# Optimization experiments

Measured on AMD Instinct MI355X. Metric: run time of the kernel, lower is better.

## Reference

```python
import jax, jax.numpy as jnp
import numpy as np

B, L, D = 2, 2048, 768
HEADS, KEY, HEAD = 12, 64, 64


def _glorot(key, shape):
    fan_in, fan_out = shape[0], shape[1]
    lim = jnp.sqrt(6.0 / (fan_in + fan_out))
    return jax.random.uniform(key, shape, jnp.float32, -lim, lim)


def setup_inputs() -> dict:
    key = jax.random.key(0)
    ks = jax.random.split(key, 8)
    return {
        "q": jax.random.normal(ks[0], (B, L, D), jnp.float32),
        "k": jax.random.normal(ks[1], (B, L, D), jnp.float32),
        "v": jax.random.normal(ks[2], (B, L, D), jnp.float32),
        "att_mask": jnp.ones((B, L), jnp.float32),
        "Wq": _glorot(ks[3], (D, HEADS * KEY)),
        "bq": jnp.zeros((HEADS * KEY,), jnp.float32),
        "Wk": _glorot(ks[4], (D, HEADS * KEY)),
        "bk": jnp.zeros((HEADS * KEY,), jnp.float32),
        "Wv": _glorot(ks[5], (D, HEADS * HEAD)),
        "bv": jnp.zeros((HEADS * HEAD,), jnp.float32),
        "Wo": _glorot(ks[6], (HEADS * HEAD, HEADS * HEAD)),
        "bo": jnp.zeros((HEADS * HEAD,), jnp.float32),
    }


def reference(q, k, v, att_mask, Wq, bq, Wk, bk, Wv, bv, Wo, bo):
    b, lq, _ = q.shape
    lk = k.shape[1]
    # att_mask [B,Lk] -> [B,Lq,Lk] via ones outer product (as in the TF code)
    mask2d = jnp.ones((b, lq, 1), jnp.float32) * att_mask[:, None, :]
    qh = (q @ Wq + bq).reshape(b, lq, HEADS, KEY)
    kh = (k @ Wk + bk).reshape(b, lk, HEADS, KEY)
    vh = (v @ Wv + bv).reshape(b, lk, HEADS, HEAD)
    # scores [B,H,Lq,Lk]
    a = jnp.einsum('binh,bjnh->bnij', qh, kh) / (KEY ** 0.5)
    a = a + (1.0 - mask2d[:, None, :, :]) * -99999.0
    a = jax.nn.softmax(a, axis=-1)
    o = jnp.einsum('bnij,bjnh->binh', a, vh).reshape(b, lq, HEADS * HEAD)
    return o @ Wo + bo
```

## Files before the change

### kernel.cpp

```cpp
#include <hip/hip_runtime.h>
#include <math.h>

#define BB 2
#define LL 2048
#define DD 768
#define NH 12
#define HD 64
#define QT 64
#define KT 32
#define NTILES (LL/KT)
#define EL (4096*768)
#define WEL (768*768)

typedef __attribute__((ext_vector_type(8))) short short8;
typedef __attribute__((ext_vector_type(4))) float f32x4;
typedef unsigned short ushortT;

union U8 { unsigned short u[8]; short8 v; };

#define MFMA(a,b,c) __builtin_amdgcn_mfma_f32_16x16x32_bf16((a),(b),(c),0,0,0)

__device__ inline unsigned short f2bf(float x) {
    unsigned int u = __float_as_uint(x);
    unsigned int r = (u + 0x7fffu + ((u >> 16) & 1u)) >> 16;
    return (unsigned short)r;
}
__device__ inline float bf2f(unsigned short s) {
    return __uint_as_float(((unsigned int)s) << 16);
}
__device__ inline void split2(float x, unsigned short& h, unsigned short& l) {
    h = f2bf(x);
    l = f2bf(x - bf2f(h));
}
__device__ inline int swz(int row) { return (((row & 7) ^ ((row >> 3) & 7)) << 4); }

__device__ inline void gl2lds16(const void* g, void* l) {
    __builtin_amdgcn_global_load_lds((__attribute__((address_space(1))) const void*)g,
                                     (__attribute__((address_space(3))) void*)l, 16, 0, 0);
}

struct SplitArgs { const float* src[3]; ushortT* dh[3]; ushortT* dl[3]; };
__global__ __launch_bounds__(256) void split_plain(SplitArgs a)
{
    const int z = blockIdx.y;
    const size_t i = ((size_t)blockIdx.x * 256 + threadIdx.x) * 8;
    const float* s = a.src[z];
    float4 v0 = *reinterpret_cast<const float4*>(s + i);
    float4 v1 = *reinterpret_cast<const float4*>(s + i + 4);
    float f[8] = {v0.x, v0.y, v0.z, v0.w, v1.x, v1.y, v1.z, v1.w};
    U8 h, l;
    #pragma unroll
    for (int j = 0; j < 8; ++j) split2(f[j], h.u[j], l.u[j]);
    *reinterpret_cast<short8*>(a.dh[z] + i) = h.v;
    *reinterpret_cast<short8*>(a.dl[z] + i) = l.v;
}

struct WArgs { const float* src[4]; ushortT* dh[4]; ushortT* dl[4]; };
__global__ __launch_bounds__(256) void split_wt(WArgs a)
{
    const int n  = blockIdx.x * 256 + threadIdx.x;
    const int k0 = blockIdx.y * 8;
    const int z  = blockIdx.z;
    const float* W = a.src[z];
    U8 h, l;
    #pragma unroll
    for (int j = 0; j < 8; ++j) {
        float x = W[(size_t)(k0 + j) * DD + n];
        split2(x, h.u[j], l.u[j]);
    }
    *reinterpret_cast<short8*>(a.dh[z] + (size_t)n * DD + k0) = h.v;
    *reinterpret_cast<short8*>(a.dl[z] + (size_t)n * DD + k0) = l.v;
}

template<int MODE>
__global__ __launch_bounds__(256) void gemm_mfma(const ushortT* __restrict__ Ah, size_t apb,
                                                 const ushortT* __restrict__ Bth, size_t bpb,
                                                 const float* __restrict__ bias,
                                                 float* __restrict__ outF,
                                                 ushortT* __restrict__ outH,
                                                 ushortT* __restrict__ outL)
{
    __shared__ ushortT As[64 * 64];
    __shared__ ushortT Bs[64 * 64];

    const int tid  = threadIdx.x;
    const int lane = tid & 63;
    const int w    = tid >> 6;
    const int g    = lane >> 4, c = lane & 15;
    const int n0   = blockIdx.x * 64;
    const int m0   = blockIdx.y * 64;

    const int srow0 = w * 16 + (lane >> 3);
    const int csrc  = (lane & 7) ^ (lane >> 3);
    const size_t plA = (csrc >= 4) ? apb : 0;
    const size_t plB = (csrc >= 4) ? bpb : 0;
    const size_t abase = (size_t)(m0 + srow0) * (DD * 2) + plA + (size_t)(csrc & 3) * 16;
    const size_t bbase = (size_t)(n0 + srow0) * (DD * 2) + plB + (size_t)(csrc & 3) * 16;

    f32x4 acc[4] = {{0,0,0,0},{0,0,0,0},{0,0,0,0},{0,0,0,0}};

    const int arow = w * 16 + c;
    const int ar7  = arow & 7;
    const int ahc  = g ^ ar7;
    const int aoff_h = arow * 64 + ahc * 8;
    const int aoff_l = arow * 64 + (ahc ^ 4) * 8;

    for (int kt = 0; kt < DD / 32; ++kt) {
        const size_t ko = (size_t)kt * 64;
        const char* asrc = (const char*)Ah  + abase + ko;
        const char* bsrc = (const char*)Bth + bbase + ko;
        gl2lds16(asrc,            &As[w * 1024]);
        gl2lds16(asrc + 8 * (DD * 2), &As[w * 1024 + 512]);
        gl2lds16(bsrc,            &Bs[w * 1024]);
        gl2lds16(bsrc + 8 * (DD * 2), &Bs[w * 1024 + 512]);
        __syncthreads();

        const short8 a_h = *reinterpret_cast<const short8*>(&As[aoff_h]);
        const short8 a_l = *reinterpret_cast<const short8*>(&As[aoff_l]);
        #pragma unroll
        for (int nf = 0; nf < 4; ++nf) {
            const int brow = nf * 16 + c;
            const int bhc  = g ^ (brow & 7);
            const short8 b_h = *reinterpret_cast<const short8*>(&Bs[brow * 64 + bhc * 8]);
            const short8 b_l = *reinterpret_cast<const short8*>(&Bs[brow * 64 + (bhc ^ 4) * 8]);
            acc[nf] = MFMA(a_h, b_h, acc[nf]);
            acc[nf] = MFMA(a_l, b_h, acc[nf]);
            acc[nf] = MFMA(a_h, b_l, acc[nf]);
        }
        __syncthreads();
    }

    #pragma unroll
    for (int nf = 0; nf < 4; ++nf) {
        const int n = n0 + nf * 16 + c;
        const float bz = bias[n];
        #pragma unroll
        for (int r = 0; r < 4; ++r) {
            const int m = m0 + w * 16 + 4 * g + r;
            const float vv = acc[nf][r] + bz;
            if (MODE == 0) {
                outF[(size_t)m * DD + n] = vv;
            } else {
                unsigned short hh, ll;
                split2(vv, hh, ll);
                outH[(size_t)m * DD + n] = hh;
                outL[(size_t)m * DD + n] = ll;
            }
        }
    }
}

__global__ __launch_bounds__(256) void attn_mfma(const ushortT* __restrict__ Qh_g,
                                                 const ushortT* __restrict__ Ql_g,
                                                 const ushortT* __restrict__ Kh_g,
                                                 const ushortT* __restrict__ Kl_g,
                                                 const ushortT* __restrict__ Vh_g,
                                                 const ushortT* __restrict__ Vl_g,
                                                 const float* __restrict__ mask,
                                                 ushortT* __restrict__ Oh_g,
                                                 ushortT* __restrict__ Ol_g)
{
    __shared__ unsigned short Kh[32 * 64];
    __shared__ unsigned short Kl[32 * 64];
    __shared__ unsigned short Vt[64 * 64];
    __shared__ unsigned short Pb[4 * 16 * 64];
    __shared__ float mterm[KT];

    const int tid = threadIdx.x;
    const int l   = tid & 63;
    const int w   = tid >> 6;
    const int g   = l >> 4;
    const int c   = l & 15;
    const int bh  = blockIdx.y;
    const int b   = bh / NH;
    const int h   = bh % NH;
    const int r0  = blockIdx.x * QT;

    short8 qh[2], ql[2];
    {
        const size_t qoff = (size_t)(b * LL + r0 + w * 16 + c) * DD + h * 64 + 8 * g;
        qh[0] = *reinterpret_cast<const short8*>(Qh_g + qoff);
        qh[1] = *reinterpret_cast<const short8*>(Qh_g + qoff + 32);
        ql[0] = *reinterpret_cast<const short8*>(Ql_g + qoff);
        ql[1] = *reinterpret_cast<const short8*>(Ql_g + qoff + 32);
    }

    f32x4 Oa[4] = {{0,0,0,0},{0,0,0,0},{0,0,0,0},{0,0,0,0}};
    float mrun[4] = {-1e30f,-1e30f,-1e30f,-1e30f};
    float lrun[4] = {0.f,0.f,0.f,0.f};

    const int skey = tid >> 3;
    const int sd0  = (tid & 7) * 8;

    for (int kt = 0; kt < NTILES; ++kt) {
        __syncthreads();
        {
            const size_t ko = (size_t)(b * LL + kt * KT + skey) * DD + h * 64 + sd0;
            const short8 hh = *reinterpret_cast<const short8*>(Kh_g + ko);
            const short8 lo = *reinterpret_cast<const short8*>(Kl_g + ko);
            const int idx = skey * 64 + (((sd0 * 2) ^ swz(skey)) >> 1);
            *reinterpret_cast<short8*>(&Kh[idx]) = hh;
            *reinterpret_cast<short8*>(&Kl[idx]) = lo;
        }
        {
            const size_t vo = (size_t)(b * LL + kt * KT + skey) * DD + h * 64 + sd0;
            U8 vh8, vl8;
            vh8.v = *reinterpret_cast<const short8*>(Vh_g + vo);
            vl8.v = *reinterpret_cast<const short8*>(Vl_g + vo);
            #pragma unroll
            for (int j = 0; j < 8; ++j) {
                const int d = sd0 + j;
                const int s = swz(d);
                Vt[d * 64 + (((2 * skey) ^ s) >> 1)]      = vh8.u[j];
                Vt[d * 64 + (((64 + 2 * skey) ^ s) >> 1)] = vl8.u[j];
            }
        }
        if (tid < KT)
            mterm[tid] = (1.0f - mask[(size_t)b * LL + kt * KT + tid]) * -99999.0f;
        __syncthreads();

        f32x4 s[2];
        #pragma unroll
        for (int th = 0; th < 2; ++th) {
            const int row = th * 16 + c;
            const int sw = swz(row);
            const short8 kh0 = *reinterpret_cast<const short8*>(&Kh[row * 64 + (((16 * g     ) ^ sw) >> 1)]);
            const short8 kh1 = *reinterpret_cast<const short8*>(&Kh[row * 64 + (((16 * g + 64) ^ sw) >> 1)]);
            const short8 kl0 = *reinterpret_cast<const short8*>(&Kl[row * 64 + (((16 * g     ) ^ sw) >> 1)]);
            const short8 kl1 = *reinterpret_cast<const short8*>(&Kl[row * 64 + (((16 * g + 64) ^ sw) >> 1)]);
            f32x4 a = {0,0,0,0};
            a = MFMA(qh[0], kh0, a); a = MFMA(qh[1], kh1, a);
            a = MFMA(ql[0], kh0, a); a = MFMA(ql[1], kh1, a);
            a = MFMA(qh[0], kl0, a); a = MFMA(qh[1], kl1, a);
            const float mt = mterm[th * 16 + c];
            #pragma unroll
            for (int r = 0; r < 4; ++r) a[r] = fmaf(a[r], 0.125f, mt);
            s[th] = a;
        }

        float pexp[2][4];
        #pragma unroll
        for (int r = 0; r < 4; ++r) {
            float tm = fmaxf(s[0][r], s[1][r]);
            #pragma unroll
            for (int o = 1; o < 16; o <<= 1) tm = fmaxf(tm, __shfl_xor(tm, o));
            const float mn = fmaxf(mrun[r], tm);
            const float scale = __expf(mrun[r] - mn);
            const float p0 = __expf(s[0][r] - mn);
            const float p1 = __expf(s[1][r] - mn);
            float rs = p0 + p1;
            #pragma unroll
            for (int o = 1; o < 16; o <<= 1) rs += __shfl_xor(rs, o);
            lrun[r] = lrun[r] * scale + rs;
            mrun[r] = mn;
            pexp[0][r] = p0; pexp[1][r] = p1;
            #pragma unroll
            for (int n = 0; n < 4; ++n) Oa[n][r] *= scale;
        }

        unsigned short* Pw = &Pb[w * 16 * 64];
        #pragma unroll
        for (int th = 0; th < 2; ++th)
            #pragma unroll
            for (int r = 0; r < 4; ++r) {
                const int row = 4 * g + r;
                const int sw2 = swz(row);
                unsigned short h_, l_;
                split2(pexp[th][r], h_, l_);
                const int keyb = 2 * (th * 16 + c);
                Pw[row * 64 + ((keyb ^ sw2) >> 1)]        = h_;
                Pw[row * 64 + (((64 + keyb) ^ sw2) >> 1)] = l_;
            }
        asm volatile("s_waitcnt lgkmcnt(0)" ::: "memory");

        {
            const int sw2 = swz(c);
            const short8 pa_h = *reinterpret_cast<const short8*>(&Pw[c * 64 + (((16 * g     ) ^ sw2) >> 1)]);
            const short8 pa_l = *reinterpret_cast<const short8*>(&Pw[c * 64 + (((64 + 16 * g) ^ sw2) >> 1)]);
            #pragma unroll
            for (int n = 0; n < 4; ++n) {
                const int vrow = 16 * n + c;
                const int sv = swz(vrow);
                const short8 vh = *reinterpret_cast<const short8*>(&Vt[vrow * 64 + (((16 * g     ) ^ sv) >> 1)]);
                const short8 vl = *reinterpret_cast<const short8*>(&Vt[vrow * 64 + (((64 + 16 * g) ^ sv) >> 1)]);
                Oa[n] = MFMA(pa_h, vh, Oa[n]);
                Oa[n] = MFMA(pa_h, vl, Oa[n]);
                Oa[n] = MFMA(pa_l, vh, Oa[n]);
            }
        }
    }

    #pragma unroll
    for (int r = 0; r < 4; ++r) {
        const float inv = 1.0f / lrun[r];
        const int row = b * LL + r0 + w * 16 + 4 * g + r;
        ushortT* oh = Oh_g + (size_t)row * DD + h * 64;
        ushortT* ol = Ol_g + (size_t)row * DD + h * 64;
        #pragma unroll
        for (int n = 0; n < 4; ++n) {
            unsigned short hh, ll;
            split2(Oa[n][r] * inv, hh, ll);
            oh[16 * n + c] = hh;
            ol[16 * n + c] = ll;
        }
    }
}

extern "C" void kernel_launch(void* const* d_in, const int* in_sizes, int n_in,
                              void* d_out, int out_size, void* d_ws, size_t ws_size,
                              hipStream_t stream)
{
    const float* q    = (const float*)d_in[0];
    const float* k    = (const float*)d_in[1];
    const float* v    = (const float*)d_in[2];
    const float* amask= (const float*)d_in[3];
    const float* Wq   = (const float*)d_in[4];
    const float* bq   = (const float*)d_in[5];
    const float* Wk   = (const float*)d_in[6];
    const float* bk   = (const float*)d_in[7];
    const float* Wv   = (const float*)d_in[8];
    const float* bv   = (const float*)d_in[9];
    const float* Wo   = (const float*)d_in[10];
    const float* bo   = (const float*)d_in[11];
    float* out = (float*)d_out;

    ushortT* W0 = (ushortT*)d_ws;
    ushortT* qh = W0;            ushortT* ql = W0 + (size_t)EL;
    ushortT* kh = W0 + 2*(size_t)EL;  ushortT* kl = W0 + 3*(size_t)EL;
    ushortT* vh = W0 + 4*(size_t)EL;  ushortT* vl = W0 + 5*(size_t)EL;
    ushortT* wb = W0 + 6*(size_t)EL;
    ushortT* wqh = wb;            ushortT* wql = wb + (size_t)WEL;
    ushortT* wkh = wb + 2*(size_t)WEL; ushortT* wkl = wb + 3*(size_t)WEL;
    ushortT* wvh = wb + 4*(size_t)WEL; ushortT* wvl = wb + 5*(size_t)WEL;
    ushortT* woh = wb + 6*(size_t)WEL; ushortT* wol = wb + 7*(size_t)WEL;
    ushortT* pb = wb + 8*(size_t)WEL;
    ushortT* Qph = pb;            ushortT* Qpl = pb + (size_t)EL;
    ushortT* Kph = pb + 2*(size_t)EL;  ushortT* Kpl = pb + 3*(size_t)EL;
    ushortT* Vph = pb + 4*(size_t)EL;  ushortT* Vpl = pb + 5*(size_t)EL;
    ushortT* Oh = W0;             ushortT* Ol = W0 + (size_t)EL;

    const size_t APB = (size_t)EL * 2;
    const size_t WPB = (size_t)WEL * 2;

    SplitArgs sa;
    sa.src[0] = q; sa.src[1] = k; sa.src[2] = v;
    sa.dh[0] = qh; sa.dh[1] = kh; sa.dh[2] = vh;
    sa.dl[0] = ql; sa.dl[1] = kl; sa.dl[2] = vl;
    split_plain<<<dim3(EL / 2048, 3), 256, 0, stream>>>(sa);

    WArgs wa;
    wa.src[0] = Wq; wa.src[1] = Wk; wa.src[2] = Wv; wa.src[3] = Wo;
    wa.dh[0] = wqh; wa.dh[1] = wkh; wa.dh[2] = wvh; wa.dh[3] = woh;
    wa.dl[0] = wql; wa.dl[1] = wkl; wa.dl[2] = wvl; wa.dl[3] = wol;
    split_wt<<<dim3(3, 96, 4), 256, 0, stream>>>(wa);

    dim3 ggrid(DD / 64, 4096 / 64);
    gemm_mfma<1><<<ggrid, 256, 0, stream>>>(qh, APB, wqh, WPB, bq, nullptr, Qph, Qpl);
    gemm_mfma<1><<<ggrid, 256, 0, stream>>>(kh, APB, wkh, WPB, bk, nullptr, Kph, Kpl);
    gemm_mfma<1><<<ggrid, 256, 0, stream>>>(vh, APB, wvh, WPB, bv, nullptr, Vph, Vpl);

    dim3 agrid(LL / QT, BB * NH);
    attn_mfma<<<agrid, 256, 0, stream>>>(Qph, Qpl, Kph, Kpl, Vph, Vpl, amask, Oh, Ol);

    gemm_mfma<0><<<ggrid, 256, 0, stream>>>(Oh, APB, woh, WPB, bo, out, nullptr, nullptr);
}
```

Before: 410.7 us.

## Rewrite attention with 32x32 MFMA, register-resident P, and fold softmax scale into Wq

The attention kernel now uses 32x32x16 bf16 MFMA with two waves of 32 query rows each. The probability matrix stays in registers and is redistributed with lane shuffles instead of being staged through LDS. K tiles are loaded directly into LDS with global_load_lds, and the 1/sqrt(d) factor is folded into the Wq split and the bq bias, which removes the per-score scale. Each block now has fewer threads (128), which can lower occupancy and latency hiding, and per-lane register use for the accumulators grows.

```diff
diff --git a/kernel.cpp b/kernel.cpp
--- a/kernel.cpp
+++ b/kernel.cpp
@@ -6,19 +6,20 @@
 #define DD 768
 #define NH 12
 #define HD 64
-#define QT 64
-#define KT 32
-#define NTILES (LL/KT)
 #define EL (4096*768)
 #define WEL (768*768)
 
 typedef __attribute__((ext_vector_type(8))) short short8;
 typedef __attribute__((ext_vector_type(4))) float f32x4;
+typedef __attribute__((ext_vector_type(16))) float f32x16;
+typedef __attribute__((ext_vector_type(4))) unsigned int u32x4;
 typedef unsigned short ushortT;
 
 union U8 { unsigned short u[8]; short8 v; };
-
-#define MFMA(a,b,c) __builtin_amdgcn_mfma_f32_16x16x32_bf16((a),(b),(c),0,0,0)
+union UB { u32x4 u; short8 v; };
+
+#define MFMA(a,b,c)   __builtin_amdgcn_mfma_f32_16x16x32_bf16((a),(b),(c),0,0,0)
+#define MFMA32(a,b,c) __builtin_amdgcn_mfma_f32_32x32x16_bf16((a),(b),(c),0,0,0)
 
 __device__ inline unsigned short f2bf(float x) {
     unsigned int u = __float_as_uint(x);
@@ -55,17 +56,18 @@
     *reinterpret_cast<short8*>(a.dl[z] + i) = l.v;
 }
 
-struct WArgs { const float* src[4]; ushortT* dh[4]; ushortT* dl[4]; };
+struct WArgs { const float* src[4]; ushortT* dh[4]; ushortT* dl[4]; float scale[4]; };
 __global__ __launch_bounds__(256) void split_wt(WArgs a)
 {
     const int n  = blockIdx.x * 256 + threadIdx.x;
     const int k0 = blockIdx.y * 8;
     const int z  = blockIdx.z;
     const float* W = a.src[z];
+    const float sc = a.scale[z];
     U8 h, l;
     #pragma unroll
     for (int j = 0; j < 8; ++j) {
-        float x = W[(size_t)(k0 + j) * DD + n];
+        float x = W[(size_t)(k0 + j) * DD + n] * sc;
         split2(x, h.u[j], l.u[j]);
     }
     *reinterpret_cast<short8*>(a.dh[z] + (size_t)n * DD + k0) = h.v;
@@ -75,7 +77,7 @@
 template<int MODE>
 __global__ __launch_bounds__(256) void gemm_mfma(const ushortT* __restrict__ Ah, size_t apb,
                                                  const ushortT* __restrict__ Bth, size_t bpb,
-                                                 const float* __restrict__ bias,
+                                                 const float* __restrict__ bias, float bscale,
                                                  float* __restrict__ outF,
                                                  ushortT* __restrict__ outH,
                                                  ushortT* __restrict__ outL)
@@ -100,8 +102,7 @@
     f32x4 acc[4] = {{0,0,0,0},{0,0,0,0},{0,0,0,0},{0,0,0,0}};
 
     const int arow = w * 16 + c;
-    const int ar7  = arow & 7;
-    const int ahc  = g ^ ar7;
+    const int ahc  = g ^ (arow & 7);
     const int aoff_h = arow * 64 + ahc * 8;
     const int aoff_l = arow * 64 + (ahc ^ 4) * 8;
 
@@ -109,9 +110,9 @@
         const size_t ko = (size_t)kt * 64;
         const char* asrc = (const char*)Ah  + abase + ko;
         const char* bsrc = (const char*)Bth + bbase + ko;
-        gl2lds16(asrc,            &As[w * 1024]);
+        gl2lds16(asrc,                &As[w * 1024]);
         gl2lds16(asrc + 8 * (DD * 2), &As[w * 1024 + 512]);
-        gl2lds16(bsrc,            &Bs[w * 1024]);
+        gl2lds16(bsrc,                &Bs[w * 1024]);
         gl2lds16(bsrc + 8 * (DD * 2), &Bs[w * 1024 + 512]);
         __syncthreads();
 
@@ -133,7 +134,7 @@
     #pragma unroll
     for (int nf = 0; nf < 4; ++nf) {
         const int n = n0 + nf * 16 + c;
-        const float bz = bias[n];
+        const float bz = bias[n] * bscale;
         #pragma unroll
         for (int r = 0; r < 4; ++r) {
             const int m = m0 + w * 16 + 4 * g + r;
@@ -150,7 +151,7 @@
     }
 }
 
-__global__ __launch_bounds__(256) void attn_mfma(const ushortT* __restrict__ Qh_g,
+__global__ __launch_bounds__(128) void attn_mfma(const ushortT* __restrict__ Qh_g,
                                                  const ushortT* __restrict__ Ql_g,
                                                  const ushortT* __restrict__ Kh_g,
                                                  const ushortT* __restrict__ Kl_g,
@@ -160,150 +161,163 @@
                                                  ushortT* __restrict__ Oh_g,
                                                  ushortT* __restrict__ Ol_g)
 {
-    __shared__ unsigned short Kh[32 * 64];
-    __shared__ unsigned short Kl[32 * 64];
-    __shared__ unsigned short Vt[64 * 64];
-    __shared__ unsigned short Pb[4 * 16 * 64];
-    __shared__ float mterm[KT];
-
-    const int tid = threadIdx.x;
-    const int l   = tid & 63;
-    const int w   = tid >> 6;
-    const int g   = l >> 4;
-    const int c   = l & 15;
-    const int bh  = blockIdx.y;
-    const int b   = bh / NH;
-    const int h   = bh % NH;
-    const int r0  = blockIdx.x * QT;
-
-    short8 qh[2], ql[2];
+    __shared__ ushortT Kh[32 * 64];
+    __shared__ ushortT Kl[32 * 64];
+    __shared__ ushortT Vt[64 * 64];
+    __shared__ float mterm[32];
+
+    const int tid  = threadIdx.x;
+    const int lane = tid & 63;
+    const int w    = tid >> 6;
+    const int qc   = lane & 31;
+    const int h5   = lane >> 5;
+    const int bh   = blockIdx.y;
+    const int b    = bh / NH;
+    const int h    = bh % NH;
+    const int r0   = blockIdx.x * 64;
+    const int qrow = r0 + w * 32 + qc;
+
+    short8 qbh[4], qbl[4];
     {
-        const size_t qoff = (size_t)(b * LL + r0 + w * 16 + c) * DD + h * 64 + 8 * g;
-        qh[0] = *reinterpret_cast<const short8*>(Qh_g + qoff);
-        qh[1] = *reinterpret_cast<const short8*>(Qh_g + qoff + 32);
-        ql[0] = *reinterpret_cast<const short8*>(Ql_g + qoff);
-        ql[1] = *reinterpret_cast<const short8*>(Ql_g + qoff + 32);
-    }
-
-    f32x4 Oa[4] = {{0,0,0,0},{0,0,0,0},{0,0,0,0},{0,0,0,0}};
-    float mrun[4] = {-1e30f,-1e30f,-1e30f,-1e30f};
-    float lrun[4] = {0.f,0.f,0.f,0.f};
-
-    const int skey = tid >> 3;
-    const int sd0  = (tid & 7) * 8;
-
-    for (int kt = 0; kt < NTILES; ++kt) {
+        const size_t qoff = (size_t)(b * LL + qrow) * DD + h * 64;
+        #pragma unroll
+        for (int ks = 0; ks < 4; ++ks) {
+            const int d0 = 8 * h5 + 16 * ks;
+            qbh[ks] = *reinterpret_cast<const short8*>(Qh_g + qoff + d0);
+            qbl[ks] = *reinterpret_cast<const short8*>(Ql_g + qoff + d0);
+        }
+    }
+
+    f32x16 Oa[2];
+    #pragma unroll
+    for (int m = 0; m < 2; ++m)
+        #pragma unroll
+        for (int r = 0; r < 16; ++r) Oa[m][r] = 0.f;
+    float mrun = -1e30f, lrun = 0.f;
+
+    const int skey = tid >> 2;
+    const int sd0v = (tid & 3) * 16;
+    ushortT* kdst = w ? Kl : Kh;
+    const ushortT* ksrcp = w ? Kl_g : Kh_g;
+    const int krow_l = lane >> 3;
+    const int kcsrc  = (lane & 7) ^ krow_l;
+
+    for (int kt = 0; kt < LL / 32; ++kt) {
         __syncthreads();
         {
-            const size_t ko = (size_t)(b * LL + kt * KT + skey) * DD + h * 64 + sd0;
-            const short8 hh = *reinterpret_cast<const short8*>(Kh_g + ko);
-            const short8 lo = *reinterpret_cast<const short8*>(Kl_g + ko);
-            const int idx = skey * 64 + (((sd0 * 2) ^ swz(skey)) >> 1);
-            *reinterpret_cast<short8*>(&Kh[idx]) = hh;
-            *reinterpret_cast<short8*>(&Kl[idx]) = lo;
+            const size_t kbase = (size_t)(b * LL + kt * 32 + krow_l) * DD + h * 64 + kcsrc * 8;
+            #pragma unroll
+            for (int t = 0; t < 4; ++t)
+                gl2lds16(ksrcp + kbase + (size_t)(8 * t) * DD, kdst + t * 512);
         }
         {
-            const size_t vo = (size_t)(b * LL + kt * KT + skey) * DD + h * 64 + sd0;
-            U8 vh8, vl8;
-            vh8.v = *reinterpret_cast<const short8*>(Vh_g + vo);
-            vl8.v = *reinterpret_cast<const short8*>(Vl_g + vo);
+            const size_t vo = (size_t)(b * LL + kt * 32 + skey) * DD + h * 64 + sd0v;
+            U8 a0, a1, b0, b1;
+            a0.v = *reinterpret_cast<const short8*>(Vh_g + vo);
+            a1.v = *reinterpret_cast<const short8*>(Vh_g + vo + 8);
+            b0.v = *reinterpret_cast<const short8*>(Vl_g + vo);
+            b1.v = *reinterpret_cast<const short8*>(Vl_g + vo + 8);
             #pragma unroll
             for (int j = 0; j < 8; ++j) {
-                const int d = sd0 + j;
-                const int s = swz(d);
-                Vt[d * 64 + (((2 * skey) ^ s) >> 1)]      = vh8.u[j];
-                Vt[d * 64 + (((64 + 2 * skey) ^ s) >> 1)] = vl8.u[j];
+                int d = sd0v + j; int s = swz(d);
+                Vt[d * 64 + (((2 * skey) ^ s) >> 1)]      = a0.u[j];
+                Vt[d * 64 + (((64 + 2 * skey) ^ s) >> 1)] = b0.u[j];
+                d = sd0v + 8 + j; s = swz(d);
+                Vt[d * 64 + (((2 * skey) ^ s) >> 1)]      = a1.u[j];
+                Vt[d * 64 + (((64 + 2 * skey) ^ s) >> 1)] = b1.u[j];
             }
         }
-        if (tid < KT)
-            mterm[tid] = (1.0f - mask[(size_t)b * LL + kt * KT + tid]) * -99999.0f;
+        if (tid < 32)
+            mterm[tid] = (1.0f - mask[(size_t)b * LL + kt * 32 + tid]) * -99999.0f;
         __syncthreads();
 
-        f32x4 s[2];
-        #pragma unroll
-        for (int th = 0; th < 2; ++th) {
-            const int row = th * 16 + c;
-            const int sw = swz(row);
-            const short8 kh0 = *reinterpret_cast<const short8*>(&Kh[row * 64 + (((16 * g     ) ^ sw) >> 1)]);
-            const short8 kh1 = *reinterpret_cast<const short8*>(&Kh[row * 64 + (((16 * g + 64) ^ sw) >> 1)]);
-            const short8 kl0 = *reinterpret_cast<const short8*>(&Kl[row * 64 + (((16 * g     ) ^ sw) >> 1)]);
-            const short8 kl1 = *reinterpret_cast<const short8*>(&Kl[row * 64 + (((16 * g + 64) ^ sw) >> 1)]);
-            f32x4 a = {0,0,0,0};
-            a = MFMA(qh[0], kh0, a); a = MFMA(qh[1], kh1, a);
-            a = MFMA(ql[0], kh0, a); a = MFMA(ql[1], kh1, a);
-            a = MFMA(qh[0], kl0, a); a = MFMA(qh[1], kl1, a);
-            const float mt = mterm[th * 16 + c];
+        f32x16 sa;
+        #pragma unroll
+        for (int r = 0; r < 16; ++r) sa[r] = 0.f;
+        #pragma unroll
+        for (int ks = 0; ks < 4; ++ks) {
+            const int ch = (h5 + 2 * ks) ^ (qc & 7);
+            const short8 kfh = *reinterpret_cast<const short8*>(&Kh[qc * 64 + ch * 8]);
+            const short8 kfl = *reinterpret_cast<const short8*>(&Kl[qc * 64 + ch * 8]);
+            sa = MFMA32(kfh, qbh[ks], sa);
+            sa = MFMA32(kfl, qbh[ks], sa);
+            sa = MFMA32(kfh, qbl[ks], sa);
+        }
+
+        float sm[16];
+        #pragma unroll
+        for (int r = 0; r < 16; ++r)
+            sm[r] = sa[r] + mterm[(r & 3) + 8 * (r >> 2) + 4 * h5];
+        float tm = sm[0];
+        #pragma unroll
+        for (int r = 1; r < 16; ++r) tm = fmaxf(tm, sm[r]);
+        tm = fmaxf(tm, __shfl_xor(tm, 32));
+        const float mn = fmaxf(mrun, tm);
+        const float scale = __expf(mrun - mn);
+        float p[16];
+        float rs = 0.f;
+        #pragma unroll
+        for (int r = 0; r < 16; ++r) { p[r] = __expf(sm[r] - mn); rs += p[r]; }
+        rs += __shfl_xor(rs, 32);
+        lrun = lrun * scale + rs;
+        mrun = mn;
+        #pragma unroll
+        for (int m = 0; m < 2; ++m)
             #pragma unroll
-            for (int r = 0; r < 4; ++r) a[r] = fmaf(a[r], 0.125f, mt);
-            s[th] = a;
-        }
-
-        float pexp[2][4];
-        #pragma unroll
-        for (int r = 0; r < 4; ++r) {
-            float tm = fmaxf(s[0][r], s[1][r]);
+            for (int r = 0; r < 16; ++r) Oa[m][r] *= scale;
+
+        unsigned int pkh[8], pkl[8], xph[8], xpl[8];
+        #pragma unroll
+        for (int s2 = 0; s2 < 8; ++s2) {
+            unsigned short h0, l0, h1, l1;
+            split2(p[2 * s2],     h0, l0);
+            split2(p[2 * s2 + 1], h1, l1);
+            pkh[s2] = (unsigned int)h0 | ((unsigned int)h1 << 16);
+            pkl[s2] = (unsigned int)l0 | ((unsigned int)l1 << 16);
+            xph[s2] = __shfl_xor(pkh[s2], 32);
+            xpl[s2] = __shfl_xor(pkl[s2], 32);
+        }
+        UB pbh[2], pbl[2];
+        if (h5 == 0) {
+            pbh[0].u = (u32x4){pkh[0], pkh[1], xph[0], xph[1]};
+            pbl[0].u = (u32x4){pkl[0], pkl[1], xpl[0], xpl[1]};
+            pbh[1].u = (u32x4){pkh[4], pkh[5], xph[4], xph[5]};
+            pbl[1].u = (u32x4){pkl[4], pkl[5], xpl[4], xpl[5]};
+        } else {
+            pbh[0].u = (u32x4){xph[2], xph[3], pkh[2], pkh[3]};
+            pbl[0].u = (u32x4){xpl[2], xpl[3], pkl[2], pkl[3]};
+            pbh[1].u = (u32x4){xph[6], xph[7], pkh[6], pkh[7]};
+            pbl[1].u = (u32x4){xpl[6], xpl[7], pkl[6], pkl[7]};
+        }
+
+        #pragma unroll
+        for (int m = 0; m < 2; ++m) {
+            const int d  = qc + 32 * m;
+            const int sv = swz(d);
             #pragma unroll
-            for (int o = 1; o < 16; o <<= 1) tm = fmaxf(tm, __shfl_xor(tm, o));
-            const float mn = fmaxf(mrun[r], tm);
-            const float scale = __expf(mrun[r] - mn);
-            const float p0 = __expf(s[0][r] - mn);
-            const float p1 = __expf(s[1][r] - mn);
-            float rs = p0 + p1;
-            #pragma unroll
-            for (int o = 1; o < 16; o <<= 1) rs += __shfl_xor(rs, o);
-            lrun[r] = lrun[r] * scale + rs;
-            mrun[r] = mn;
-            pexp[0][r] = p0; pexp[1][r] = p1;
-            #pragma unroll
-            for (int n = 0; n < 4; ++n) Oa[n][r] *= scale;
-        }
-
-        unsigned short* Pw = &Pb[w * 16 * 64];
-        #pragma unroll
-        for (int th = 0; th < 2; ++th)
-            #pragma unroll
-            for (int r = 0; r < 4; ++r) {
-                const int row = 4 * g + r;
-                const int sw2 = swz(row);
-                unsigned short h_, l_;
-                split2(pexp[th][r], h_, l_);
-                const int keyb = 2 * (th * 16 + c);
-                Pw[row * 64 + ((keyb ^ sw2) >> 1)]        = h_;
-                Pw[row * 64 + (((64 + keyb) ^ sw2) >> 1)] = l_;
+            for (int ks2 = 0; ks2 < 2; ++ks2) {
+                const int bc = 16 * h5 + 32 * ks2;
+                const short8 vfh = *reinterpret_cast<const short8*>(&Vt[d * 64 + ((bc ^ sv) >> 1)]);
+                const short8 vfl = *reinterpret_cast<const short8*>(&Vt[d * 64 + (((64 + bc) ^ sv) >> 1)]);
+                Oa[m] = MFMA32(vfh, pbh[ks2].v, Oa[m]);
+                Oa[m] = MFMA32(vfl, pbh[ks2].v, Oa[m]);
+                Oa[m] = MFMA32(vfh, pbl[ks2].v, Oa[m]);
             }
-        asm volatile("s_waitcnt lgkmcnt(0)" ::: "memory");
-
-        {
-            const int sw2 = swz(c);
-            const short8 pa_h = *reinterpret_cast<const short8*>(&Pw[c * 64 + (((16 * g     ) ^ sw2) >> 1)]);
-            const short8 pa_l = *reinterpret_cast<const short8*>(&Pw[c * 64 + (((64 + 16 * g) ^ sw2) >> 1)]);
-            #pragma unroll
-            for (int n = 0; n < 4; ++n) {
-                const int vrow = 16 * n + c;
-                const int sv = swz(vrow);
-                const short8 vh = *reinterpret_cast<const short8*>(&Vt[vrow * 64 + (((16 * g     ) ^ sv) >> 1)]);
-                const short8 vl = *reinterpret_cast<const short8*>(&Vt[vrow * 64 + (((64 + 16 * g) ^ sv) >> 1)]);
-                Oa[n] = MFMA(pa_h, vh, Oa[n]);
-                Oa[n] = MFMA(pa_h, vl, Oa[n]);
-                Oa[n] = MFMA(pa_l, vh, Oa[n]);
-            }
-        }
-    }
-
-    #pragma unroll
-    for (int r = 0; r < 4; ++r) {
-        const float inv = 1.0f / lrun[r];
-        const int row = b * LL + r0 + w * 16 + 4 * g + r;
-        ushortT* oh = Oh_g + (size_t)row * DD + h * 64;
-        ushortT* ol = Ol_g + (size_t)row * DD + h * 64;
-        #pragma unroll
-        for (int n = 0; n < 4; ++n) {
+        }
+    }
+
+    const float inv = 1.0f / lrun;
+    const size_t obase = (size_t)(b * LL + qrow) * DD + h * 64;
+    #pragma unroll
+    for (int m = 0; m < 2; ++m)
+        #pragma unroll
+        for (int r = 0; r < 16; ++r) {
+            const int d = (r & 3) + 8 * (r >> 2) + 4 * h5 + 32 * m;
             unsigned short hh, ll;
-            split2(Oa[n][r] * inv, hh, ll);
-            oh[16 * n + c] = hh;
-            ol[16 * n + c] = ll;
-        }
-    }
+            split2(Oa[m][r] * inv, hh, ll);
+            Oh_g[obase + d] = hh;
+            Ol_g[obase + d] = ll;
+        }
 }
 
 extern "C" void kernel_launch(void* const* d_in, const int* in_sizes, int n_in,
@@ -325,19 +339,19 @@
     float* out = (float*)d_out;
 
     ushortT* W0 = (ushortT*)d_ws;
-    ushortT* qh = W0;            ushortT* ql = W0 + (size_t)EL;
+    ushortT* qh = W0;                 ushortT* ql = W0 + (size_t)EL;
     ushortT* kh = W0 + 2*(size_t)EL;  ushortT* kl = W0 + 3*(size_t)EL;
     ushortT* vh = W0 + 4*(size_t)EL;  ushortT* vl = W0 + 5*(size_t)EL;
     ushortT* wb = W0 + 6*(size_t)EL;
-    ushortT* wqh = wb;            ushortT* wql = wb + (size_t)WEL;
+    ushortT* wqh = wb;                 ushortT* wql = wb + (size_t)WEL;
     ushortT* wkh = wb + 2*(size_t)WEL; ushortT* wkl = wb + 3*(size_t)WEL;
     ushortT* wvh = wb + 4*(size_t)WEL; ushortT* wvl = wb + 5*(size_t)WEL;
     ushortT* woh = wb + 6*(size_t)WEL; ushortT* wol = wb + 7*(size_t)WEL;
     ushortT* pb = wb + 8*(size_t)WEL;
-    ushortT* Qph = pb;            ushortT* Qpl = pb + (size_t)EL;
+    ushortT* Qph = pb;                 ushortT* Qpl = pb + (size_t)EL;
     ushortT* Kph = pb + 2*(size_t)EL;  ushortT* Kpl = pb + 3*(size_t)EL;
     ushortT* Vph = pb + 4*(size_t)EL;  ushortT* Vpl = pb + 5*(size_t)EL;
-    ushortT* Oh = W0;             ushortT* Ol = W0 + (size_t)EL;
+    ushortT* Oh = W0;                  ushortT* Ol = W0 + (size_t)EL;
 
     const size_t APB = (size_t)EL * 2;
     const size_t WPB = (size_t)WEL * 2;
@@ -352,15 +366,16 @@
     wa.src[0] = Wq; wa.src[1] = Wk; wa.src[2] = Wv; wa.src[3] = Wo;
     wa.dh[0] = wqh; wa.dh[1] = wkh; wa.dh[2] = wvh; wa.dh[3] = woh;
     wa.dl[0] = wql; wa.dl[1] = wkl; wa.dl[2] = wvl; wa.dl[3] = wol;
+    wa.scale[0] = 0.125f; wa.scale[1] = 1.f; wa.scale[2] = 1.f; wa.scale[3] = 1.f;
     split_wt<<<dim3(3, 96, 4), 256, 0, stream>>>(wa);
 
     dim3 ggrid(DD / 64, 4096 / 64);
-    gemm_mfma<1><<<ggrid, 256, 0, stream>>>(qh, APB, wqh, WPB, bq, nullptr, Qph, Qpl);
-    gemm_mfma<1><<<ggrid, 256, 0, stream>>>(kh, APB, wkh, WPB, bk, nullptr, Kph, Kpl);
-    gemm_mfma<1><<<ggrid, 256, 0, stream>>>(vh, APB, wvh, WPB, bv, nullptr, Vph, Vpl);
-
-    dim3 agrid(LL / QT, BB * NH);
-    attn_mfma<<<agrid, 256, 0, stream>>>(Qph, Qpl, Kph, Kpl, Vph, Vpl, amask, Oh, Ol);
-
-    gemm_mfma<0><<<ggrid, 256, 0, stream>>>(Oh, APB, woh, WPB, bo, out, nullptr, nullptr);
-}
+    gemm_mfma<1><<<ggrid, 256, 0, stream>>>(qh, APB, wqh, WPB, bq, 0.125f, nullptr, Qph, Qpl);
+    gemm_mfma<1><<<ggrid, 256, 0, stream>>>(kh, APB, wkh, WPB, bk, 1.0f,   nullptr, Kph, Kpl);
+    gemm_mfma<1><<<ggrid, 256, 0, stream>>>(vh, APB, wvh, WPB, bv, 1.0f,   nullptr, Vph, Vpl);
+
+    dim3 agrid(LL / 64, BB * NH);
+    attn_mfma<<<agrid, 128, 0, stream>>>(Qph, Qpl, Kph, Kpl, Vph, Vpl, amask, Oh, Ol);
+
+    gemm_mfma<0><<<ggrid, 256, 0, stream>>>(Oh, APB, woh, WPB, bo, 1.0f, out, nullptr, nullptr);
+}
```

Result: faster. 388.0 us (-5.5%).
